# Kernel optimization log

Hardware: AMD Instinct MI355X
Metric: run time of the kernel (lower is better)

## Reference

```python
import jax, jax.numpy as jnp
import numpy as np

N_USERS = 100000
M_ITEMS = 50000
N = N_USERS + M_ITEMS
D = 64
NNZ = 4800000
N_LAYERS = 3


def spmm(idx, val, x):
    # sparse COO (idx[0]=rows, idx[1]=cols) @ dense x : gather-scale-scatter
    rows, cols = idx[0], idx[1]
    return jax.ops.segment_sum(val[:, None] * x[cols], rows, num_segments=N)


def propagate(idx, val, emb0):
    # LightGCN propagation: mean over layer-0..n_layers embeddings
    embs = [emb0]
    e = emb0
    for _ in range(N_LAYERS):
        e = spmm(idx, val, e)
        embs.append(e)
    return jnp.mean(jnp.stack(embs, axis=1), axis=1)  # [N, D]


def setup_inputs() -> dict:
    key = jax.random.key(0)
    ks = jax.random.split(key, 10)
    return {
        "emb_im": 0.1 * jax.random.normal(ks[0], (N, D), jnp.float32),
        "emb_q": 0.1 * jax.random.normal(ks[1], (N, D), jnp.float32),
        "emb_p": 0.1 * jax.random.normal(ks[2], (N, D), jnp.float32),
        "g_im_idx": jax.random.randint(ks[3], (2, NNZ), 0, N, jnp.int32),
        "g_im_val": jax.random.uniform(ks[4], (NNZ,), jnp.float32) / 32.0,
        "g_q_idx": jax.random.randint(ks[5], (2, NNZ), 0, N, jnp.int32),
        "g_q_val": jax.random.uniform(ks[6], (NNZ,), jnp.float32) / 32.0,
        "g_p_idx": jax.random.randint(ks[7], (2, NNZ), 0, N, jnp.int32),
        "g_p_val": jax.random.uniform(ks[8], (NNZ,), jnp.float32) / 32.0,
        "add_weight": jnp.ones((3,), jnp.float32),
    }


def reference(emb_im, emb_q, emb_p, g_im_idx, g_im_val, g_q_idx, g_q_val,
              g_p_idx, g_p_val, add_weight):
    out_im = propagate(g_im_idx, g_im_val, emb_im)
    out_q = propagate(g_q_idx, g_q_val, emb_q)
    out_p = propagate(g_p_idx, g_p_val, emb_p)
    # weighted_add over factors: sum_f w_f * out_f ; users/items split is a
    # row split of this combined [N, D] matrix
    stacked = jnp.stack([out_im, out_q, out_p], axis=0)  # [3, N, D]
    combined = jnp.sum(stacked * add_weight[:, None, None], axis=0)  # [N, D]
    return combined  # rows [:N_USERS] = users, rows [N_USERS:] = items
```

## Files before the change

kernel.cpp:

```cpp
#include <hip/hip_runtime.h>

#define N_TOTAL 150000
#define DIM 64
#define RPB 293
#define NBUCK 512
#define MAGIC 14658592u
#define CAP 10368
#define CHUNK 8192

typedef float v2f __attribute__((ext_vector_type(2)));

__global__ void fill_bcur_kernel(int* __restrict__ bcur) {
    int t = blockIdx.x * 256 + threadIdx.x;
    if (t < NBUCK) bcur[t] = t * CAP;
}

__global__ void bin_kernel(const int* __restrict__ idx, const float* __restrict__ val,
                           int* __restrict__ bcur, unsigned* __restrict__ bcs,
                           unsigned short* __restrict__ brl, int nnz) {
    __shared__ unsigned scs[CHUNK];
    __shared__ unsigned srow[CHUNK];
    __shared__ int lcnt[NBUCK];
    __shared__ int lstart[NBUCK + 1];
    __shared__ int gbase[NBUCK];
    int t = threadIdx.x;
    int base = blockIdx.x * CHUNK;
    int nEdges = min(CHUNK, nnz - base);
    lcnt[t] = 0;
    __syncthreads();
    unsigned mycs[16];
    int myrow[16], myb[16];
    #pragma unroll
    for (int i = 0; i < 16; ++i) {
        int e = base + t + i * 512;
        if (e < nnz) {
            int r = idx[e];
            int b = (int)__umulhi((unsigned)r, MAGIC);
            myb[i] = b;
            myrow[i] = r;
            unsigned v14 = (__float_as_uint(val[e]) + 0x20000u) >> 18;
            mycs[i] = ((unsigned)idx[nnz + e] << 14) | v14;
            atomicAdd(&lcnt[b], 1);
        } else {
            myb[i] = -1;
        }
    }
    __syncthreads();
    int c = lcnt[t];
    lstart[t] = c;
    __syncthreads();
    for (int off = 1; off < 512; off <<= 1) {
        int x = (t >= off) ? lstart[t - off] : 0;
        __syncthreads();
        lstart[t] += x;
        __syncthreads();
    }
    int incl = lstart[t];
    __syncthreads();
    lstart[t] = incl - c;
    if (t == 511) lstart[512] = incl;
    gbase[t] = c ? atomicAdd(&bcur[t], c) : 0;
    lcnt[t] = 0;
    __syncthreads();
    #pragma unroll
    for (int i = 0; i < 16; ++i) {
        int b = myb[i];
        if (b >= 0) {
            int o = atomicAdd(&lcnt[b], 1);
            int p = lstart[b] + o;
            scs[p] = mycs[i];
            srow[p] = (unsigned)myrow[i];
        }
    }
    __syncthreads();
    for (int p = t; p < nEdges; p += 512) {
        int r = (int)srow[p];
        int b = (int)__umulhi((unsigned)r, MAGIC);
        int dst = gbase[b] + (p - lstart[b]);
        if (dst < (b + 1) * CAP) {
            bcs[dst] = scs[p];
            brl[dst] = (unsigned short)(r - b * RPB);
        }
    }
}

__global__ void scatterc_kernel(const unsigned* __restrict__ bcs,
                                const unsigned short* __restrict__ brl,
                                const int* __restrict__ bcur,
                                int* __restrict__ rlo, int* __restrict__ rhi,
                                unsigned* __restrict__ cs) {
    __shared__ int hist[RPB];
    __shared__ int ssc[256];
    int b = blockIdx.x, t = threadIdx.x;
    int s = b * CAP, e = min(bcur[b], s + CAP);
    for (int i = t; i < RPB; i += 256) hist[i] = 0;
    __syncthreads();
    for (int k = s + t; k < e; k += 256)
        atomicAdd(&hist[brl[k]], 1);
    __syncthreads();
    int i0 = 2 * t;
    int c0 = (i0 < RPB) ? hist[i0] : 0;
    int c1 = (i0 + 1 < RPB) ? hist[i0 + 1] : 0;
    int s2 = c0 + c1;
    ssc[t] = s2;
    __syncthreads();
    for (int off = 1; off < 256; off <<= 1) {
        int x = (t >= off) ? ssc[t - off] : 0;
        __syncthreads();
        ssc[t] += x;
        __syncthreads();
    }
    int excl = ssc[t] - s2;
    __syncthreads();
    int base0 = s + excl, base1 = s + excl + c0;
    if (i0 < RPB) {
        int row = b * RPB + i0;
        if (row < N_TOTAL) { rlo[row] = base0; rhi[row] = base0 + c0; }
        hist[i0] = base0;
    }
    if (i0 + 1 < RPB) {
        int row = b * RPB + i0 + 1;
        if (row < N_TOTAL) { rlo[row] = base1; rhi[row] = base1 + c1; }
        hist[i0 + 1] = base1;
    }
    __syncthreads();
    for (int k = s + t; k < e; k += 256) {
        int rl_ = brl[k];
        int o = atomicAdd(&hist[rl_], 1);
        cs[o] = bcs[k];
    }
}

__global__ void conv_fp8_kernel(const float* __restrict__ x, uint2* __restrict__ y, int n8) {
    int i = blockIdx.x * blockDim.x + threadIdx.x;
    if (i >= n8) return;
    const float4* x4 = reinterpret_cast<const float4*>(x);
    float4 a = x4[2 * i], b = x4[2 * i + 1];
    int p0 = __builtin_amdgcn_cvt_pk_fp8_f32(a.x * 64.f, a.y * 64.f, 0, false);
    p0 = __builtin_amdgcn_cvt_pk_fp8_f32(a.z * 64.f, a.w * 64.f, p0, true);
    int p1 = __builtin_amdgcn_cvt_pk_fp8_f32(b.x * 64.f, b.y * 64.f, 0, false);
    p1 = __builtin_amdgcn_cvt_pk_fp8_f32(b.z * 64.f, b.w * 64.f, p1, true);
    uint2 o;
    o.x = (unsigned)p0;
    o.y = (unsigned)p1;
    y[i] = o;
}

__global__ void spmm_fp8_kernel(const int* __restrict__ rlo, const int* __restrict__ rhi,
                                const unsigned* __restrict__ cs, const uint2* __restrict__ x2,
                                uint2* __restrict__ y2, int nrows) {
    int gid = blockIdx.x * blockDim.x + threadIdx.x;
    int row = gid >> 6;
    int lane = gid & 63;
    if (row >= nrows) return;
    int s = rlo[row], e = rhi[row];
    int q = lane >> 3, sub = lane & 7;
    float ac[8], bc[8];
    #pragma unroll
    for (int d = 0; d < 8; ++d) { ac[d] = 0.f; bc[d] = 0.f; }
    int k = s + q;
    for (; k + 8 < e; k += 16) {
        unsigned ed0 = cs[k], ed1 = cs[k + 8];
        uint2 g0 = x2[((size_t)(ed0 >> 14) << 3) + sub];
        uint2 g1 = x2[((size_t)(ed1 >> 14) << 3) + sub];
        float v0 = __uint_as_float((ed0 & 0x3FFFu) << 18);
        float v1 = __uint_as_float((ed1 & 0x3FFFu) << 18);
        v2f l0 = __builtin_amdgcn_cvt_pk_f32_fp8((int)g0.x, false);
        v2f h0 = __builtin_amdgcn_cvt_pk_f32_fp8((int)g0.x, true);
        v2f l1 = __builtin_amdgcn_cvt_pk_f32_fp8((int)g0.y, false);
        v2f h1 = __builtin_amdgcn_cvt_pk_f32_fp8((int)g0.y, true);
        ac[0] += v0 * l0.x; ac[1] += v0 * l0.y; ac[2] += v0 * h0.x; ac[3] += v0 * h0.y;
        ac[4] += v0 * l1.x; ac[5] += v0 * l1.y; ac[6] += v0 * h1.x; ac[7] += v0 * h1.y;
        v2f l2 = __builtin_amdgcn_cvt_pk_f32_fp8((int)g1.x, false);
        v2f h2 = __builtin_amdgcn_cvt_pk_f32_fp8((int)g1.x, true);
        v2f l3 = __builtin_amdgcn_cvt_pk_f32_fp8((int)g1.y, false);
        v2f h3 = __builtin_amdgcn_cvt_pk_f32_fp8((int)g1.y, true);
        bc[0] += v1 * l2.x; bc[1] += v1 * l2.y; bc[2] += v1 * h2.x; bc[3] += v1 * h2.y;
        bc[4] += v1 * l3.x; bc[5] += v1 * l3.y; bc[6] += v1 * h3.x; bc[7] += v1 * h3.y;
    }
    for (; k < e; k += 8) {
        unsigned ed = cs[k];
        uint2 g = x2[((size_t)(ed >> 14) << 3) + sub];
        float vv = __uint_as_float((ed & 0x3FFFu) << 18);
        v2f l0 = __builtin_amdgcn_cvt_pk_f32_fp8((int)g.x, false);
        v2f h0 = __builtin_amdgcn_cvt_pk_f32_fp8((int)g.x, true);
        v2f l1 = __builtin_amdgcn_cvt_pk_f32_fp8((int)g.y, false);
        v2f h1 = __builtin_amdgcn_cvt_pk_f32_fp8((int)g.y, true);
        ac[0] += vv * l0.x; ac[1] += vv * l0.y; ac[2] += vv * h0.x; ac[3] += vv * h0.y;
        ac[4] += vv * l1.x; ac[5] += vv * l1.y; ac[6] += vv * h1.x; ac[7] += vv * h1.y;
    }
    #pragma unroll
    for (int d = 0; d < 8; ++d) {
        float a = ac[d] + bc[d];
        a += __shfl_xor(a, 8);
        a += __shfl_xor(a, 16);
        a += __shfl_xor(a, 32);
        ac[d] = a;
    }
    if (q == 0) {
        int p0 = __builtin_amdgcn_cvt_pk_fp8_f32(ac[0], ac[1], 0, false);
        p0 = __builtin_amdgcn_cvt_pk_fp8_f32(ac[2], ac[3], p0, true);
        int p1 = __builtin_amdgcn_cvt_pk_fp8_f32(ac[4], ac[5], 0, false);
        p1 = __builtin_amdgcn_cvt_pk_fp8_f32(ac[6], ac[7], p1, true);
        uint2 o;
        o.x = (unsigned)p0;
        o.y = (unsigned)p1;
        y2[((size_t)row << 3) + sub] = o;
    }
}

__device__ inline float4 dec_sum3(const unsigned* __restrict__ T, int i, int nwords) {
    unsigned a = T[i], b = T[i + nwords], c = T[i + 2 * nwords];
    v2f alo = __builtin_amdgcn_cvt_pk_f32_fp8((int)a, false);
    v2f ahi = __builtin_amdgcn_cvt_pk_f32_fp8((int)a, true);
    v2f blo = __builtin_amdgcn_cvt_pk_f32_fp8((int)b, false);
    v2f bhi = __builtin_amdgcn_cvt_pk_f32_fp8((int)b, true);
    v2f clo = __builtin_amdgcn_cvt_pk_f32_fp8((int)c, false);
    v2f chi = __builtin_amdgcn_cvt_pk_f32_fp8((int)c, true);
    float4 r;
    r.x = alo.x + blo.x + clo.x;
    r.y = alo.y + blo.y + clo.y;
    r.z = ahi.x + bhi.x + chi.x;
    r.w = ahi.y + bhi.y + chi.y;
    return r;
}

__global__ void combine3_kernel(const float* __restrict__ e0, const float* __restrict__ e1,
                                const float* __restrict__ e2, const unsigned* __restrict__ t0,
                                const unsigned* __restrict__ t1, const unsigned* __restrict__ t2,
                                const float* __restrict__ w, float* __restrict__ out,
                                int nwords) {
    int i = blockIdx.x * blockDim.x + threadIdx.x;
    if (i >= nwords) return;
    const float kInv = 1.f / 64.f;
    float c0 = w[0] * 0.25f, c1 = w[1] * 0.25f, c2 = w[2] * 0.25f;
    float4 ev0 = reinterpret_cast<const float4*>(e0)[i];
    float4 ev1 = reinterpret_cast<const float4*>(e1)[i];
    float4 ev2 = reinterpret_cast<const float4*>(e2)[i];
    float4 s0 = dec_sum3(t0, i, nwords);
    float4 s1 = dec_sum3(t1, i, nwords);
    float4 s2 = dec_sum3(t2, i, nwords);
    float4 o;
    o.x = c0 * (ev0.x + kInv * s0.x) + c1 * (ev1.x + kInv * s1.x) + c2 * (ev2.x + kInv * s2.x);
    o.y = c0 * (ev0.y + kInv * s0.y) + c1 * (ev1.y + kInv * s1.y) + c2 * (ev2.y + kInv * s2.y);
    o.z = c0 * (ev0.z + kInv * s0.z) + c1 * (ev1.z + kInv * s1.z) + c2 * (ev2.z + kInv * s2.z);
    o.w = c0 * (ev0.w + kInv * s0.w) + c1 * (ev1.w + kInv * s1.w) + c2 * (ev2.w + kInv * s2.w);
    reinterpret_cast<float4*>(out)[i] = o;
}

template <bool FIRST>
__global__ void combine_kernel(const float* __restrict__ emb, const unsigned* __restrict__ T,
                               const float* __restrict__ w, int f, float* __restrict__ out,
                               int nwords) {
    int i = blockIdx.x * blockDim.x + threadIdx.x;
    if (i >= nwords) return;
    float c = w[f] * 0.25f;
    const float kInv = 1.f / 64.f;
    float4 e = reinterpret_cast<const float4*>(emb)[i];
    float4 s = dec_sum3(T, i, nwords);
    float4 o;
    o.x = c * (e.x + s.x * kInv);
    o.y = c * (e.y + s.y * kInv);
    o.z = c * (e.z + s.z * kInv);
    o.w = c * (e.w + s.w * kInv);
    float4* o4 = reinterpret_cast<float4*>(out) + i;
    if (FIRST) {
        *o4 = o;
    } else {
        float4 cv = *o4;
        cv.x += o.x; cv.y += o.y; cv.z += o.z; cv.w += o.w;
        *o4 = cv;
    }
}

extern "C" void kernel_launch(void* const* d_in, const int* in_sizes, int n_in,
                              void* d_out, int out_size, void* d_ws, size_t ws_size,
                              hipStream_t stream) {
    const float* emb[3]  = {(const float*)d_in[0], (const float*)d_in[1], (const float*)d_in[2]};
    const int*   gidx[3] = {(const int*)d_in[3],   (const int*)d_in[5],   (const int*)d_in[7]};
    const float* gval[3] = {(const float*)d_in[4], (const float*)d_in[6], (const float*)d_in[8]};
    const float* w = (const float*)d_in[9];
    float* out = (float*)d_out;

    const int nnz = in_sizes[4];
    const size_t bufElems = (size_t)N_TOTAL * DIM;
    const size_t fp8Bytes = bufElems;
    const size_t capElems = (size_t)NBUCK * CAP;

    char* base = (char*)d_ws;
    unsigned*       bcs  = (unsigned*)base;
    unsigned*       emb8 = (unsigned*)base;
    unsigned short* brl  = (unsigned short*)(base + capElems * 4);
    unsigned*       cs   = (unsigned*)(base + capElems * 6);
    int*            rlo  = (int*)(base + capElems * 10);
    int*            rhi  = rlo + N_TOTAL;
    int*            bcur = rhi + N_TOTAL;
    char*           tab  = base + capElems * 10 + (size_t)2 * N_TOTAL * 4 + 4096;
    const size_t needFused = (tab - base) + (size_t)9 * fp8Bytes;
    const bool fused = ws_size >= needFused;

    const int n8 = (int)(bufElems / 8);
    const int nwords = (int)(bufElems / 4);
    dim3 cvtGrid((n8 + 255) / 256);
    dim3 cmbGrid((nwords + 255) / 256);
    dim3 chunkGrid((nnz + CHUNK - 1) / CHUNK);
    dim3 rowGrid((unsigned)(((size_t)N_TOTAL * 64 + 255) / 256));

    for (int f = 0; f < 3; ++f) {
        unsigned* A8 = (unsigned*)(tab + (size_t)(fused ? 3 * f + 0 : 0) * fp8Bytes);
        unsigned* B8 = (unsigned*)(tab + (size_t)(fused ? 3 * f + 1 : 1) * fp8Bytes);
        unsigned* C8 = (unsigned*)(tab + (size_t)(fused ? 3 * f + 2 : 2) * fp8Bytes);

        fill_bcur_kernel<<<2, 256, 0, stream>>>(bcur);
        bin_kernel<<<chunkGrid, 512, 0, stream>>>(gidx[f], gval[f], bcur, bcs, brl, nnz);
        scatterc_kernel<<<NBUCK, 256, 0, stream>>>(bcs, brl, bcur, rlo, rhi, cs);

        conv_fp8_kernel<<<cvtGrid, 256, 0, stream>>>(emb[f], (uint2*)emb8, n8);

        spmm_fp8_kernel<<<rowGrid, 256, 0, stream>>>(rlo, rhi, cs, (const uint2*)emb8,
                                                     (uint2*)A8, N_TOTAL);
        spmm_fp8_kernel<<<rowGrid, 256, 0, stream>>>(rlo, rhi, cs, (const uint2*)A8,
                                                     (uint2*)B8, N_TOTAL);
        spmm_fp8_kernel<<<rowGrid, 256, 0, stream>>>(rlo, rhi, cs, (const uint2*)B8,
                                                     (uint2*)C8, N_TOTAL);

        if (!fused) {
            if (f == 0)
                combine_kernel<true><<<cmbGrid, 256, 0, stream>>>(emb[f], A8, w, f, out, nwords);
            else
                combine_kernel<false><<<cmbGrid, 256, 0, stream>>>(emb[f], A8, w, f, out, nwords);
        }
    }

    if (fused) {
        const unsigned* t0 = (const unsigned*)(tab + (size_t)0 * fp8Bytes);
        const unsigned* t1 = (const unsigned*)(tab + (size_t)3 * fp8Bytes);
        const unsigned* t2 = (const unsigned*)(tab + (size_t)6 * fp8Bytes);
        combine3_kernel<<<cmbGrid, 256, 0, stream>>>(emb[0], emb[1], emb[2], t0, t1, t2,
                                                     w, out, nwords);
    }
}
```

Measured before the change: 986.9 us.

## Fuse row scatter, fp8 conversion and combine into one kernel; shrink bin chunks

```diff
diff --git a/kernel.cpp b/kernel.cpp
--- a/kernel.cpp
+++ b/kernel.cpp
@@ -6,7 +6,7 @@
 #define NBUCK 512
 #define MAGIC 14658592u
 #define CAP 10368
-#define CHUNK 8192
+#define CHUNK 4096
 
 typedef float v2f __attribute__((ext_vector_type(2)));
 
@@ -23,16 +23,17 @@
     __shared__ int lcnt[NBUCK];
     __shared__ int lstart[NBUCK + 1];
     __shared__ int gbase[NBUCK];
+    __shared__ int ssc[256];
     int t = threadIdx.x;
     int base = blockIdx.x * CHUNK;
     int nEdges = min(CHUNK, nnz - base);
-    lcnt[t] = 0;
+    lcnt[t] = 0; lcnt[t + 256] = 0;
     __syncthreads();
     unsigned mycs[16];
     int myrow[16], myb[16];
     #pragma unroll
     for (int i = 0; i < 16; ++i) {
-        int e = base + t + i * 512;
+        int e = base + t + i * 256;
         if (e < nnz) {
             int r = idx[e];
             int b = (int)__umulhi((unsigned)r, MAGIC);
@@ -46,21 +47,25 @@
         }
     }
     __syncthreads();
-    int c = lcnt[t];
-    lstart[t] = c;
-    __syncthreads();
-    for (int off = 1; off < 512; off <<= 1) {
-        int x = (t >= off) ? lstart[t - off] : 0;
+    int i0 = 2 * t;
+    int c0 = lcnt[i0], c1 = lcnt[i0 + 1];
+    int s2 = c0 + c1;
+    ssc[t] = s2;
+    __syncthreads();
+    for (int off = 1; off < 256; off <<= 1) {
+        int x = (t >= off) ? ssc[t - off] : 0;
         __syncthreads();
-        lstart[t] += x;
+        ssc[t] += x;
         __syncthreads();
     }
-    int incl = lstart[t];
-    __syncthreads();
-    lstart[t] = incl - c;
-    if (t == 511) lstart[512] = incl;
-    gbase[t] = c ? atomicAdd(&bcur[t], c) : 0;
-    lcnt[t] = 0;
+    int incl = ssc[t];
+    int excl = incl - s2;
+    lstart[i0] = excl;
+    lstart[i0 + 1] = excl + c0;
+    if (t == 255) lstart[NBUCK] = incl;
+    gbase[i0]     = c0 ? atomicAdd(&bcur[i0], c0) : 0;
+    gbase[i0 + 1] = c1 ? atomicAdd(&bcur[i0 + 1], c1) : 0;
+    lcnt[i0] = 0; lcnt[i0 + 1] = 0;
     __syncthreads();
     #pragma unroll
     for (int i = 0; i < 16; ++i) {
@@ -73,7 +78,7 @@
         }
     }
     __syncthreads();
-    for (int p = t; p < nEdges; p += 512) {
+    for (int p = t; p < nEdges; p += 256) {
         int r = (int)srow[p];
         int b = (int)__umulhi((unsigned)r, MAGIC);
         int dst = gbase[b] + (p - lstart[b]);
@@ -84,14 +89,15 @@
     }
 }
 
-__global__ void scatterc_kernel(const unsigned* __restrict__ bcs,
-                                const unsigned short* __restrict__ brl,
-                                const int* __restrict__ bcur,
-                                int* __restrict__ rlo, int* __restrict__ rhi,
-                                unsigned* __restrict__ cs) {
+
+__device__ void scatterc_body(int b, const unsigned* __restrict__ bcs,
+                              const unsigned short* __restrict__ brl,
+                              int* __restrict__ bcur,
+                              int* __restrict__ rlo, int* __restrict__ rhi,
+                              unsigned* __restrict__ cs2) {
     __shared__ int hist[RPB];
     __shared__ int ssc[256];
-    int b = blockIdx.x, t = threadIdx.x;
+    int t = threadIdx.x;
     int s = b * CAP, e = min(bcur[b], s + CAP);
     for (int i = t; i < RPB; i += 256) hist[i] = 0;
     __syncthreads();
@@ -127,26 +133,112 @@
     for (int k = s + t; k < e; k += 256) {
         int rl_ = brl[k];
         int o = atomicAdd(&hist[rl_], 1);
-        cs[o] = bcs[k];
-    }
-}
-
-__global__ void conv_fp8_kernel(const float* __restrict__ x, uint2* __restrict__ y, int n8) {
+        cs2[o] = bcs[k];
+    }
+    __syncthreads();
+    if (t == 0) bcur[b] = s;
+}
+
+__device__ void conv_body(int i, const float* __restrict__ x, unsigned* __restrict__ y,
+                          int nwords) {
+    if (i >= nwords) return;
+    int row = i >> 4, w_ = i & 15;
+    const float* xr = x + ((size_t)row << 6) + w_;
+    int p = __builtin_amdgcn_cvt_pk_fp8_f32(xr[0] * 64.f, xr[16] * 64.f, 0, false);
+    p = __builtin_amdgcn_cvt_pk_fp8_f32(xr[32] * 64.f, xr[48] * 64.f, p, true);
+    y[i] = (unsigned)p;
+}
+
+__device__ inline float4 dec_sum3(const unsigned* __restrict__ T, int i, int nwords) {
+    unsigned a = T[i], b = T[i + nwords], c = T[i + 2 * nwords];
+    v2f alo = __builtin_amdgcn_cvt_pk_f32_fp8((int)a, false);
+    v2f ahi = __builtin_amdgcn_cvt_pk_f32_fp8((int)a, true);
+    v2f blo = __builtin_amdgcn_cvt_pk_f32_fp8((int)b, false);
+    v2f bhi = __builtin_amdgcn_cvt_pk_f32_fp8((int)b, true);
+    v2f clo = __builtin_amdgcn_cvt_pk_f32_fp8((int)c, false);
+    v2f chi = __builtin_amdgcn_cvt_pk_f32_fp8((int)c, true);
+    float4 r;
+    r.x = alo.x + blo.x + clo.x;
+    r.y = alo.y + blo.y + clo.y;
+    r.z = ahi.x + bhi.x + chi.x;
+    r.w = ahi.y + bhi.y + chi.y;
+    return r;
+}
+
+__device__ void combine_body(int i, const float* __restrict__ emb,
+                             const unsigned* __restrict__ T, float c,
+                             float* __restrict__ out, int nwords, bool first) {
+    if (i >= nwords) return;
+    const float kInv = 1.f / 64.f;
+    int r = i >> 4, wd = i & 15;
+    size_t base = ((size_t)r << 6) + wd;
+    float4 s = dec_sum3(T, i, nwords);
+    float v0 = c * (emb[base] + kInv * s.x);
+    float v1 = c * (emb[base + 16] + kInv * s.y);
+    float v2 = c * (emb[base + 32] + kInv * s.z);
+    float v3 = c * (emb[base + 48] + kInv * s.w);
+    if (first) {
+        out[base] = v0; out[base + 16] = v1; out[base + 32] = v2; out[base + 48] = v3;
+    } else {
+        out[base] += v0; out[base + 16] += v1; out[base + 32] += v2; out[base + 48] += v3;
+    }
+}
+
+__global__ void scv_kernel(const unsigned* __restrict__ bcs,
+                           const unsigned short* __restrict__ brl,
+                           int* __restrict__ bcur, int* __restrict__ rlo,
+                           int* __restrict__ rhi, unsigned* __restrict__ cs2,
+                           const float* __restrict__ embf, unsigned* __restrict__ emb8,
+                           const float* __restrict__ embp, const unsigned* __restrict__ Tp,
+                           const float* __restrict__ w, int fprev, float* __restrict__ out,
+                           int nwords, int nCvt) {
+    int b = blockIdx.x;
+    if (b < NBUCK) {
+        scatterc_body(b, bcs, brl, bcur, rlo, rhi, cs2);
+        return;
+    }
+    b -= NBUCK;
+    if (b < nCvt) {
+        conv_body(b * 256 + (int)threadIdx.x, embf, emb8, nwords);
+        return;
+    }
+    b -= nCvt;
+    combine_body(b * 256 + (int)threadIdx.x, embp, Tp, w[fprev] * 0.25f, out, nwords,
+                 fprev == 0);
+}
+
+__global__ void combine_kernel(const float* __restrict__ emb, const unsigned* __restrict__ T,
+                               const float* __restrict__ w, int f, float* __restrict__ out,
+                               int nwords) {
+    combine_body(blockIdx.x * 256 + (int)threadIdx.x, emb, T, w[f] * 0.25f, out, nwords,
+                 false);
+}
+
+__global__ void combine3_kernel(const float* __restrict__ e0, const float* __restrict__ e1,
+                                const float* __restrict__ e2, const unsigned* __restrict__ t0,
+                                const unsigned* __restrict__ t1, const unsigned* __restrict__ t2,
+                                const float* __restrict__ w, float* __restrict__ out,
+                                int nwords) {
     int i = blockIdx.x * blockDim.x + threadIdx.x;
-    if (i >= n8) return;
-    const float4* x4 = reinterpret_cast<const float4*>(x);
-    float4 a = x4[2 * i], b = x4[2 * i + 1];
-    int p0 = __builtin_amdgcn_cvt_pk_fp8_f32(a.x * 64.f, a.y * 64.f, 0, false);
-    p0 = __builtin_amdgcn_cvt_pk_fp8_f32(a.z * 64.f, a.w * 64.f, p0, true);
-    int p1 = __builtin_amdgcn_cvt_pk_fp8_f32(b.x * 64.f, b.y * 64.f, 0, false);
-    p1 = __builtin_amdgcn_cvt_pk_fp8_f32(b.z * 64.f, b.w * 64.f, p1, true);
-    uint2 o;
-    o.x = (unsigned)p0;
-    o.y = (unsigned)p1;
-    y[i] = o;
-}
-
-__global__ void spmm_fp8_kernel(const int* __restrict__ rlo, const int* __restrict__ rhi,
+    if (i >= nwords) return;
+    const float kInv = 1.f / 64.f;
+    float c0 = w[0] * 0.25f, c1 = w[1] * 0.25f, c2 = w[2] * 0.25f;
+    int r = i >> 4, wd = i & 15;
+    size_t base = ((size_t)r << 6) + wd;
+    float4 s0 = dec_sum3(t0, i, nwords);
+    float4 s1 = dec_sum3(t1, i, nwords);
+    float4 s2 = dec_sum3(t2, i, nwords);
+    out[base]      = c0 * (e0[base]      + kInv * s0.x) + c1 * (e1[base]      + kInv * s1.x)
+                   + c2 * (e2[base]      + kInv * s2.x);
+    out[base + 16] = c0 * (e0[base + 16] + kInv * s0.y) + c1 * (e1[base + 16] + kInv * s1.y)
+                   + c2 * (e2[base + 16] + kInv * s2.y);
+    out[base + 32] = c0 * (e0[base + 32] + kInv * s0.z) + c1 * (e1[base + 32] + kInv * s1.z)
+                   + c2 * (e2[base + 32] + kInv * s2.z);
+    out[base + 48] = c0 * (e0[base + 48] + kInv * s0.w) + c1 * (e1[base + 48] + kInv * s1.w)
+                   + c2 * (e2[base + 48] + kInv * s2.w);
+}
+
+__global__ void spmm_reg_kernel(const int* __restrict__ rlo, const int* __restrict__ rhi,
                                 const unsigned* __restrict__ cs, const uint2* __restrict__ x2,
                                 uint2* __restrict__ y2, int nrows) {
     int gid = blockIdx.x * blockDim.x + threadIdx.x;
@@ -209,70 +301,6 @@
     }
 }
 
-__device__ inline float4 dec_sum3(const unsigned* __restrict__ T, int i, int nwords) {
-    unsigned a = T[i], b = T[i + nwords], c = T[i + 2 * nwords];
-    v2f alo = __builtin_amdgcn_cvt_pk_f32_fp8((int)a, false);
-    v2f ahi = __builtin_amdgcn_cvt_pk_f32_fp8((int)a, true);
-    v2f blo = __builtin_amdgcn_cvt_pk_f32_fp8((int)b, false);
-    v2f bhi = __builtin_amdgcn_cvt_pk_f32_fp8((int)b, true);
-    v2f clo = __builtin_amdgcn_cvt_pk_f32_fp8((int)c, false);
-    v2f chi = __builtin_amdgcn_cvt_pk_f32_fp8((int)c, true);
-    float4 r;
-    r.x = alo.x + blo.x + clo.x;
-    r.y = alo.y + blo.y + clo.y;
-    r.z = ahi.x + bhi.x + chi.x;
-    r.w = ahi.y + bhi.y + chi.y;
-    return r;
-}
-
-__global__ void combine3_kernel(const float* __restrict__ e0, const float* __restrict__ e1,
-                                const float* __restrict__ e2, const unsigned* __restrict__ t0,
-                                const unsigned* __restrict__ t1, const unsigned* __restrict__ t2,
-                                const float* __restrict__ w, float* __restrict__ out,
-                                int nwords) {
-    int i = blockIdx.x * blockDim.x + threadIdx.x;
-    if (i >= nwords) return;
-    const float kInv = 1.f / 64.f;
-    float c0 = w[0] * 0.25f, c1 = w[1] * 0.25f, c2 = w[2] * 0.25f;
-    float4 ev0 = reinterpret_cast<const float4*>(e0)[i];
-    float4 ev1 = reinterpret_cast<const float4*>(e1)[i];
-    float4 ev2 = reinterpret_cast<const float4*>(e2)[i];
-    float4 s0 = dec_sum3(t0, i, nwords);
-    float4 s1 = dec_sum3(t1, i, nwords);
-    float4 s2 = dec_sum3(t2, i, nwords);
-    float4 o;
-    o.x = c0 * (ev0.x + kInv * s0.x) + c1 * (ev1.x + kInv * s1.x) + c2 * (ev2.x + kInv * s2.x);
-    o.y = c0 * (ev0.y + kInv * s0.y) + c1 * (ev1.y + kInv * s1.y) + c2 * (ev2.y + kInv * s2.y);
-    o.z = c0 * (ev0.z + kInv * s0.z) + c1 * (ev1.z + kInv * s1.z) + c2 * (ev2.z + kInv * s2.z);
-    o.w = c0 * (ev0.w + kInv * s0.w) + c1 * (ev1.w + kInv * s1.w) + c2 * (ev2.w + kInv * s2.w);
-    reinterpret_cast<float4*>(out)[i] = o;
-}
-
-template <bool FIRST>
-__global__ void combine_kernel(const float* __restrict__ emb, const unsigned* __restrict__ T,
-                               const float* __restrict__ w, int f, float* __restrict__ out,
-                               int nwords) {
-    int i = blockIdx.x * blockDim.x + threadIdx.x;
-    if (i >= nwords) return;
-    float c = w[f] * 0.25f;
-    const float kInv = 1.f / 64.f;
-    float4 e = reinterpret_cast<const float4*>(emb)[i];
-    float4 s = dec_sum3(T, i, nwords);
-    float4 o;
-    o.x = c * (e.x + s.x * kInv);
-    o.y = c * (e.y + s.y * kInv);
-    o.z = c * (e.z + s.z * kInv);
-    o.w = c * (e.w + s.w * kInv);
-    float4* o4 = reinterpret_cast<float4*>(out) + i;
-    if (FIRST) {
-        *o4 = o;
-    } else {
-        float4 cv = *o4;
-        cv.x += o.x; cv.y += o.y; cv.z += o.z; cv.w += o.w;
-        *o4 = cv;
-    }
-}
-
 extern "C" void kernel_launch(void* const* d_in, const int* in_sizes, int n_in,
                               void* d_out, int out_size, void* d_ws, size_t ws_size,
                               hipStream_t stream) {
@@ -284,59 +312,61 @@
 
     const int nnz = in_sizes[4];
     const size_t bufElems = (size_t)N_TOTAL * DIM;
-    const size_t fp8Bytes = bufElems;
+    const int nwords = (int)(bufElems / 4);
+    const size_t fp8Bytes = (size_t)nwords * 4;
     const size_t capElems = (size_t)NBUCK * CAP;
 
     char* base = (char*)d_ws;
     unsigned*       bcs  = (unsigned*)base;
-    unsigned*       emb8 = (unsigned*)base;
     unsigned short* brl  = (unsigned short*)(base + capElems * 4);
-    unsigned*       cs   = (unsigned*)(base + capElems * 6);
-    int*            rlo  = (int*)(base + capElems * 10);
+    unsigned*       cs2  = (unsigned*)(base + capElems * 6);
+    unsigned*       emb8 = (unsigned*)(base + capElems * 10);
+    int*            rlo  = (int*)(base + capElems * 10 + fp8Bytes);
     int*            rhi  = rlo + N_TOTAL;
     int*            bcur = rhi + N_TOTAL;
-    char*           tab  = base + capElems * 10 + (size_t)2 * N_TOTAL * 4 + 4096;
-    const size_t needFused = (tab - base) + (size_t)9 * fp8Bytes;
+    char*           tab  = (char*)(bcur + NBUCK + 64);
+    const size_t needFused = (size_t)(tab - base) + (size_t)9 * fp8Bytes;
     const bool fused = ws_size >= needFused;
 
-    const int n8 = (int)(bufElems / 8);
-    const int nwords = (int)(bufElems / 4);
-    dim3 cvtGrid((n8 + 255) / 256);
+    const int nCvt = (nwords + 255) / 256;
+    dim3 binGrid((nnz + CHUNK - 1) / CHUNK);
+    dim3 rowGrid((unsigned)(((size_t)N_TOTAL * 64 + 255) / 256));
     dim3 cmbGrid((nwords + 255) / 256);
-    dim3 chunkGrid((nnz + CHUNK - 1) / CHUNK);
-    dim3 rowGrid((unsigned)(((size_t)N_TOTAL * 64 + 255) / 256));
+
+    fill_bcur_kernel<<<2, 256, 0, stream>>>(bcur);
 
     for (int f = 0; f < 3; ++f) {
-        unsigned* A8 = (unsigned*)(tab + (size_t)(fused ? 3 * f + 0 : 0) * fp8Bytes);
-        unsigned* B8 = (unsigned*)(tab + (size_t)(fused ? 3 * f + 1 : 1) * fp8Bytes);
-        unsigned* C8 = (unsigned*)(tab + (size_t)(fused ? 3 * f + 2 : 2) * fp8Bytes);
-
-        fill_bcur_kernel<<<2, 256, 0, stream>>>(bcur);
-        bin_kernel<<<chunkGrid, 512, 0, stream>>>(gidx[f], gval[f], bcur, bcs, brl, nnz);
-        scatterc_kernel<<<NBUCK, 256, 0, stream>>>(bcs, brl, bcur, rlo, rhi, cs);
-
-        conv_fp8_kernel<<<cvtGrid, 256, 0, stream>>>(emb[f], (uint2*)emb8, n8);
-
-        spmm_fp8_kernel<<<rowGrid, 256, 0, stream>>>(rlo, rhi, cs, (const uint2*)emb8,
+        unsigned* tabF = (unsigned*)(tab + (size_t)(fused ? 3 * f : 0) * fp8Bytes);
+        unsigned* A8 = tabF;
+        unsigned* B8 = tabF + nwords;
+        unsigned* C8 = tabF + 2 * (size_t)nwords;
+
+        bin_kernel<<<binGrid, 256, 0, stream>>>(gidx[f], gval[f], bcur, bcs, brl, nnz);
+
+        int hasCmb = (!fused && f > 0) ? 1 : 0;
+        const unsigned* Tprev = (const unsigned*)tab;
+        const float* embPrev = (f > 0) ? emb[f - 1] : emb[0];
+        dim3 scvGrid(NBUCK + nCvt + (hasCmb ? nCvt : 0));
+        scv_kernel<<<scvGrid, 256, 0, stream>>>(bcs, brl, bcur, rlo, rhi, cs2,
+                                                emb[f], emb8, embPrev, Tprev,
+                                                w, f - 1, out, nwords, nCvt);
+
+        spmm_reg_kernel<<<rowGrid, 256, 0, stream>>>(rlo, rhi, cs2, (const uint2*)emb8,
                                                      (uint2*)A8, N_TOTAL);
-        spmm_fp8_kernel<<<rowGrid, 256, 0, stream>>>(rlo, rhi, cs, (const uint2*)A8,
+        spmm_reg_kernel<<<rowGrid, 256, 0, stream>>>(rlo, rhi, cs2, (const uint2*)A8,
                                                      (uint2*)B8, N_TOTAL);
-        spmm_fp8_kernel<<<rowGrid, 256, 0, stream>>>(rlo, rhi, cs, (const uint2*)B8,
+        spmm_reg_kernel<<<rowGrid, 256, 0, stream>>>(rlo, rhi, cs2, (const uint2*)B8,
                                                      (uint2*)C8, N_TOTAL);
-
-        if (!fused) {
-            if (f == 0)
-                combine_kernel<true><<<cmbGrid, 256, 0, stream>>>(emb[f], A8, w, f, out, nwords);
-            else
-                combine_kernel<false><<<cmbGrid, 256, 0, stream>>>(emb[f], A8, w, f, out, nwords);
-        }
     }
 
     if (fused) {
-        const unsigned* t0 = (const unsigned*)(tab + (size_t)0 * fp8Bytes);
-        const unsigned* t1 = (const unsigned*)(tab + (size_t)3 * fp8Bytes);
-        const unsigned* t2 = (const unsigned*)(tab + (size_t)6 * fp8Bytes);
+        const unsigned* t0 = (const unsigned*)tab;
+        const unsigned* t1 = t0 + 3 * (size_t)nwords;
+        const unsigned* t2 = t0 + 6 * (size_t)nwords;
         combine3_kernel<<<cmbGrid, 256, 0, stream>>>(emb[0], emb[1], emb[2], t0, t1, t2,
                                                      w, out, nwords);
-    }
-}
+    } else {
+        combine_kernel<<<cmbGrid, 256, 0, stream>>>(emb[2], (const unsigned*)tab, w, 2,
+                                                    out, nwords);
+    }
+}
```

New measurement: 1.073 ms. +8.7%, slower.
